# Optimization experiments

Hardware: AMD Instinct MI355X
Metric: run time of the kernel (lower is better)

The kernel has to match this reference:

```python
import jax, jax.numpy as jnp
import numpy as np
from jax import lax

EPS = 1e-5  # BatchNorm eps (inference mode: running_mean=m, running_var=v)
DN = ('NCDHW', 'OIDHW', 'NCDHW')


def _conv_bn_relu(x, W, b, g, bt, m, v, pad):
    y = lax.conv_general_dilated(x, W, window_strides=(1, 1, 1), padding=pad,
                                 dimension_numbers=DN)
    y = y + b[None, :, None, None, None]
    scale = g / jnp.sqrt(v + EPS)
    y = (y - m[None, :, None, None, None]) * scale[None, :, None, None, None] \
        + bt[None, :, None, None, None]
    return jax.nn.relu(y)


def _cal_patt(k, q, v):
    # spatial non-local attention over H*W, independently per (n, c, d)
    N, C, D, H, W = q.shape
    qf = q.reshape(N, C, D, H * W)
    kf = k.reshape(N, C, D, H * W)
    vf = v.reshape(N, C, D, H * W)
    # sigma[n,c,d,i,j] = q_i * k_j ; softmax over j ; out[j] = sum_i v_i * r_ij
    sigma = qf[..., :, None] * kf[..., None, :]          # [N,C,D,HW,HW]
    r = jax.nn.softmax(sigma, axis=-1)
    out = jnp.einsum('ncdi,ncdij->ncdj', vf, r)
    return out.reshape(N, C, D, H, W)


def _cal_datt(k, q, v):
    # temporal non-local attention over D, independently per (n, c, h, w)
    N, C, D, H, W = q.shape
    qf = jnp.transpose(q, (0, 1, 3, 4, 2))               # [N,C,H,W,D]
    kf = jnp.transpose(k, (0, 1, 3, 4, 2))
    vf = jnp.transpose(v, (0, 1, 3, 4, 2))
    sigma = qf[..., :, None] * kf[..., None, :]          # [N,C,H,W,D,D]
    r = jax.nn.softmax(sigma, axis=-1)
    out = jnp.einsum('nchwi,nchwij->nchwj', vf, r)
    return jnp.transpose(out, (0, 1, 4, 2, 3))           # back to [N,C,D,H,W]


def setup_inputs() -> dict:
    key = jax.random.key(0)
    ks = jax.random.split(key, 8)
    C, Cc = 512, 64  # features_, features_//compress
    N, D, H, W = 2, 8, 16, 16
    f32 = jnp.float32

    def bn(c):
        return (jnp.ones((c,), f32), jnp.zeros((c,), f32),
                jnp.zeros((c,), f32), jnp.ones((c,), f32))

    x = jax.random.normal(ks[0], (N, C, D, H, W), f32)
    Wq = jax.random.normal(ks[1], (Cc, C, 1, 1, 1), f32) * 0.04
    Wk = jax.random.normal(ks[2], (Cc, C, 1, 1, 1), f32) * 0.04
    Wv = jax.random.normal(ks[3], (Cc, C, 1, 1, 1), f32) * 0.04
    Ws = jax.random.normal(ks[4], (C, Cc, 3, 3, 3), f32) * 0.02
    Wd = jax.random.normal(ks[5], (C, Cc, 3, 3, 3), f32) * 0.02
    gq, btq, mq, vq = bn(Cc)
    gk, btk, mk, vk = bn(Cc)
    gv, btv, mv, vv = bn(Cc)
    gs, bts, ms, vs = bn(C)
    gd, btd, md, vd = bn(C)
    return dict(
        x=x, gama=jnp.float32(0.5),
        Wq=Wq, bq=jnp.zeros((Cc,), f32), gq=gq, btq=btq, mq=mq, vq=vq,
        Wk=Wk, bk=jnp.zeros((Cc,), f32), gk=gk, btk=btk, mk=mk, vk=vk,
        Wv=Wv, bv=jnp.zeros((Cc,), f32), gv=gv, btv=btv, mv=mv, vv=vv,
        Ws=Ws, bs=jnp.zeros((C,), f32), gs=gs, bts=bts, ms=ms, vs=vs,
        Wd=Wd, bd=jnp.zeros((C,), f32), gd=gd, btd=btd, md=md, vd=vd,
    )


def reference(x, gama,
              Wq, bq, gq, btq, mq, vq,
              Wk, bk, gk, btk, mk, vk,
              Wv, bv, gv, btv, mv, vv,
              Ws, bs, gs, bts, ms, vs,
              Wd, bd, gd, btd, md, vd):
    P0 = [(0, 0)] * 3
    P1 = [(1, 1)] * 3
    v_x = _conv_bn_relu(x, Wv, bv, gv, btv, mv, vv, P0)
    k_x = _conv_bn_relu(x, Wk, bk, gk, btk, mk, vk, P0)
    q_x = _conv_bn_relu(x, Wq, bq, gq, btq, mq, vq, P0)
    # name == 'st': both spatial and temporal attention branches
    Patt = _cal_patt(k_x, q_x, v_x)
    Patt_c = _conv_bn_relu(Patt, Ws, bs, gs, bts, ms, vs, P1)
    Datt = _cal_datt(k_x, q_x, v_x)
    Datt_c = _conv_bn_relu(Datt, Wd, bd, gd, btd, md, vd, P1)
    return gama * (Datt_c + Patt_c) + x
```

## Files before the change

### kernel.cpp

```cpp
#include <hip/hip_runtime.h>
#include <cmath>

#define EPSBN 1e-5f

namespace {
constexpr int C_IN = 512;
constexpr int CC   = 64;
constexpr int CD   = 8;
constexpr int HW   = 256;
constexpr int DHW  = CD * HW;
constexpr int QSZ  = 2 * CC * DHW;

constexpr int PG    = 18 * 18;
constexpr int GPLN  = PG * 8;
constexpr int PADSZ = 2 * 10 * 8 * GPLN;
constexpr int WTSZ  = 27 * 512 * 64;
constexpr int PSTR  = 1448;

typedef __attribute__((ext_vector_type(8))) short bf16x8;
typedef __attribute__((ext_vector_type(4))) float f32x4;
typedef __attribute__((ext_vector_type(16))) float f32x16;

typedef unsigned int u32_g __attribute__((address_space(1)));
typedef unsigned int u32_l __attribute__((address_space(3)));

__device__ inline unsigned short f2bf(float f) {
    unsigned u = __float_as_uint(f);
    return (unsigned short)((u + 0x7fffu + ((u >> 16) & 1u)) >> 16);
}
}

__global__ __launch_bounds__(256) void prep_kernel(
    const float* __restrict__ Ws, const float* __restrict__ Wd,
    const float* __restrict__ Wq, const float* __restrict__ Wk,
    const float* __restrict__ Wv,
    const float* __restrict__ bs, const float* __restrict__ gs,
    const float* __restrict__ bts, const float* __restrict__ ms,
    const float* __restrict__ vs,
    const float* __restrict__ bd, const float* __restrict__ gd,
    const float* __restrict__ btd, const float* __restrict__ md,
    const float* __restrict__ vd,
    uint4* __restrict__ pads, unsigned short* __restrict__ Wt,
    unsigned short* __restrict__ Wqkv, float2* __restrict__ BNc)
{
    int bid = blockIdx.x;
    int t = threadIdx.x;
    if (bid < 405) {
        pads[bid * 256 + t] = make_uint4(0, 0, 0, 0);
    } else if (bid < 1429) {
        int b2 = bid - 405;
        int b  = b2 >> 9;
        int co = b2 & 511;
        const float* W = b ? Wd : Ws;
        int cog = co >> 6, co_l = co & 63;
        unsigned short* o = Wt + (size_t)b * WTSZ;
        for (int k = t; k < 27 * 64; k += 256) {
            int tap = k >> 6, ci = k & 63;
            int kd = tap / 9, tapk = tap - kd * 9;
            int half = ci >> 5, cl = ci & 31;
            int cig = cl >> 4, ci16 = cl & 15;
            float w = W[((size_t)co * 64 + ci) * 27 + tap];
            int chunk = ((cog * 2 + half) * 3 + kd) * 2 + cig;
            o[(size_t)chunk * 9216 + tapk * 1024 + co_l * 16 + ci16] = f2bf(w);
        }
    } else if (bid < 1621) {
        int co = bid - 1429;
        const float* W = co < 64 ? Wq : co < 128 ? Wk : Wv;
        int c = co & 63;
        for (int ci = t; ci < 512; ci += 256)
            Wqkv[(size_t)co * 512 + ci] = f2bf(W[(size_t)c * 512 + ci]);
    } else {
        int gid = (bid - 1621) * 256 + t;
        if (gid < 1024) {
            int br = gid >> 9, co = gid & 511;
            float s, o;
            if (br == 0) {
                s = gs[co] * rsqrtf(vs[co] + EPSBN);
                o = (bs[co] - ms[co]) * s + bts[co];
            } else {
                s = gd[co] * rsqrtf(vd[co] + EPSBN);
                o = (bd[co] - md[co]) * s + btd[co];
            }
            BNc[gid] = make_float2(s, o);
        }
    }
}

__global__ __launch_bounds__(256) void qkv_gemm_kernel(
    const float* __restrict__ x, const unsigned short* __restrict__ Wqkv,
    const float* __restrict__ bq, const float* __restrict__ gq,
    const float* __restrict__ btq, const float* __restrict__ mq,
    const float* __restrict__ vq,
    const float* __restrict__ bk, const float* __restrict__ gk,
    const float* __restrict__ btk, const float* __restrict__ mk,
    const float* __restrict__ vk,
    const float* __restrict__ bv, const float* __restrict__ gv,
    const float* __restrict__ btv, const float* __restrict__ mv,
    const float* __restrict__ vv,
    float* __restrict__ outq, float* __restrict__ outk, float* __restrict__ outv)
{
    int bid = blockIdx.x;
    int n = bid >> 7, p0 = (bid & 127) * 16;

    __shared__ __align__(16) unsigned short xs[16 * 512];
    int t = threadIdx.x;

    const float* xb = x + ((size_t)n * C_IN) * DHW + p0;
#pragma unroll
    for (int pass = 0; pass < 8; ++pass) {
        int idx = pass * 256 + t;
        int ci = idx >> 2, pq = idx & 3;
        float4 v4 = *reinterpret_cast<const float4*>(xb + (size_t)ci * DHW + pq * 4);
        float arr[4] = {v4.x, v4.y, v4.z, v4.w};
#pragma unroll
        for (int u = 0; u < 4; ++u) {
            int pos = pq * 4 + u;
            int boff = pos * 1024 + ((ci * 2) ^ ((pos & 7) << 4));
            *reinterpret_cast<unsigned short*>(
                reinterpret_cast<char*>(xs) + boff) = f2bf(arr[u]);
        }
    }
    __syncthreads();

    int wid = t >> 6, lane = t & 63;
    int l15 = lane & 15, l4 = lane >> 4;
    int mh = wid * 3;
    int pos = l15;

    bf16x8 bfr[16];
    const char* xsb = reinterpret_cast<const char*>(xs) + pos * 1024;
    int swz = (pos & 7) << 4;
#pragma unroll
    for (int kk = 0; kk < 16; ++kk)
        bfr[kk] = *reinterpret_cast<const bf16x8*>(xsb + ((kk * 64 + l4 * 16) ^ swz));

    f32x4 acc[3];
#pragma unroll
    for (int i = 0; i < 3; ++i) acc[i] = (f32x4){0.f, 0.f, 0.f, 0.f};

#pragma unroll
    for (int i = 0; i < 3; ++i) {
        const unsigned short* wrow =
            Wqkv + ((size_t)(mh + i) * 16 + l15) * 512 + l4 * 8;
#pragma unroll
        for (int kk = 0; kk < 16; ++kk) {
            bf16x8 af = *reinterpret_cast<const bf16x8*>(wrow + kk * 32);
            acc[i] = __builtin_amdgcn_mfma_f32_16x16x32_bf16(af, bfr[kk], acc[i], 0, 0, 0);
        }
    }

#pragma unroll
    for (int i = 0; i < 3; ++i) {
        int mf = mh + i;
        int br = mf >> 2;
        const float* bb  = br == 0 ? bq  : br == 1 ? bk  : bv;
        const float* gg  = br == 0 ? gq  : br == 1 ? gk  : gv;
        const float* bt  = br == 0 ? btq : br == 1 ? btk : btv;
        const float* mm  = br == 0 ? mq  : br == 1 ? mk  : mv;
        const float* vvp = br == 0 ? vq  : br == 1 ? vk  : vv;
        float*       op  = br == 0 ? outq : br == 1 ? outk : outv;
        int cb = (mf & 3) * 16 + l4 * 4;
#pragma unroll
        for (int r = 0; r < 4; ++r) {
            int c = cb + r;
            float s = gg[c] * rsqrtf(vvp[c] + EPSBN);
            float val = (acc[i][r] + bb[c] - mm[c]) * s + bt[c];
            op[((size_t)(n * CC + c)) * DHW + p0 + pos] = fmaxf(val, 0.f);
        }
    }
}

__global__ __launch_bounds__(256) void att_kernel(
    const float* __restrict__ q, const float* __restrict__ k,
    const float* __restrict__ v,
    unsigned short* __restrict__ Pp, unsigned short* __restrict__ Dp)
{
    __shared__ float sk[256], sq[256], sw[256], red[4];
    int t = threadIdx.x;
    int bid = blockIdx.x;

    if (bid < 1024) {
        int n = bid >> 9, c = (bid >> 3) & 63, d = bid & 7;
        size_t base = (size_t)bid * HW;
        float kt = k[base + t];
        float qt = q[base + t];
        float vt = v[base + t];
        sk[t] = kt;
        sq[t] = qt;

        float m = kt;
#pragma unroll
        for (int off = 32; off >= 1; off >>= 1)
            m = fmaxf(m, __shfl_xor(m, off));
        if ((t & 63) == 0) red[t >> 6] = m;
        __syncthreads();
        float kmax = fmaxf(fmaxf(red[0], red[1]), fmaxf(red[2], red[3]));

        float qkm = qt * kmax;
        float d0 = 0.f, d1 = 0.f, d2 = 0.f, d3 = 0.f;
        for (int j = 0; j < 256; j += 4) {
            d0 += __expf(fmaf(qt, sk[j + 0], -qkm));
            d1 += __expf(fmaf(qt, sk[j + 1], -qkm));
            d2 += __expf(fmaf(qt, sk[j + 2], -qkm));
            d3 += __expf(fmaf(qt, sk[j + 3], -qkm));
        }
        float den = (d0 + d1) + (d2 + d3);
        sw[t] = vt / den;
        __syncthreads();

        float kjm = kt - kmax;
        float o0 = 0.f, o1 = 0.f, o2 = 0.f, o3 = 0.f;
        for (int i = 0; i < 256; i += 4) {
            o0 += sw[i + 0] * __expf(sq[i + 0] * kjm);
            o1 += sw[i + 1] * __expf(sq[i + 1] * kjm);
            o2 += sw[i + 2] * __expf(sq[i + 2] * kjm);
            o3 += sw[i + 3] * __expf(sq[i + 3] * kjm);
        }
        float o = (o0 + o1) + (o2 + o3);

        int h = t >> 4, w = t & 15;
        size_t dst = ((((size_t)(n * 10 + d + 1) * 8 + (c >> 3)) * PG)
                      + (h + 1) * 18 + (w + 1)) * 8 + (c & 7);
        Pp[dst] = f2bf(o);
    } else {
        int g = (bid - 1024) * 256 + t;
        int nc = g >> 8, hw = g & 255;
        int n = nc >> 6, c = nc & 63;
        size_t base = (size_t)nc * DHW + hw;

        float qv[8], kv[8], vv_[8];
#pragma unroll
        for (int d = 0; d < 8; ++d) {
            qv[d]  = q[base + d * HW];
            kv[d]  = k[base + d * HW];
            vv_[d] = v[base + d * HW];
        }
        float kmax = 0.f;
#pragma unroll
        for (int d = 0; d < 8; ++d) kmax = fmaxf(kmax, kv[d]);

        float wgt[8];
#pragma unroll
        for (int i = 0; i < 8; ++i) {
            float den = 0.f, qkm = qv[i] * kmax;
#pragma unroll
            for (int j = 0; j < 8; ++j)
                den += __expf(fmaf(qv[i], kv[j], -qkm));
            wgt[i] = vv_[i] / den;
        }
        int h = hw >> 4, w = hw & 15;
#pragma unroll
        for (int j = 0; j < 8; ++j) {
            float o = 0.f, kjm = kv[j] - kmax;
#pragma unroll
            for (int i = 0; i < 8; ++i)
                o += wgt[i] * __expf(qv[i] * kjm);
            size_t dst = ((((size_t)(n * 10 + j + 1) * 8 + (c >> 3)) * PG)
                          + (h + 1) * 18 + (w + 1)) * 8 + (c & 7);
            Dp[dst] = f2bf(o);
        }
    }
}

__global__ __launch_bounds__(256, 1) void conv_fused_kernel(
    const unsigned short* __restrict__ Pp, const unsigned short* __restrict__ Dp,
    const unsigned short* __restrict__ Wt,
    const float2* __restrict__ BNc,
    const float* __restrict__ x, const float* __restrict__ gama,
    float* __restrict__ out)
{
    int bid = blockIdx.x;
    int cog = bid & 7;
    int pgb = (bid >> 3) & 1;
    int sl  = bid >> 4;
    int n = sl >> 3, d = sl & 7;

    __shared__ __align__(16) unsigned short lds_in[2 * 12 * PSTR];
    __shared__ __align__(16) unsigned short lds_w[2 * 18432];

    int t = threadIdx.x;
    int wid = t >> 6, lane = t & 63;
    int ph = wid & 1, br = wid >> 1;
    int col  = lane & 31;
    int wcol = lane & 15;
    int hl   = (lane >> 4) & 1;
    int ks   = lane >> 5;

    f32x16 acc[2][2];
#pragma unroll
    for (int m = 0; m < 2; ++m)
#pragma unroll
        for (int p = 0; p < 2; ++p)
#pragma unroll
            for (int r = 0; r < 16; ++r)
                acc[m][p][r] = 0.f;

#define DMAW(c_) do {                                                         \
    const int ch_ = (((cog * 2 + ((c_) / 6)) * 3 + (((c_) % 6) >> 1)) * 2     \
                     + ((c_) & 1)) * 9216;                                    \
    _Pragma("unroll")                                                         \
    for (int j = 0; j < 9; ++j) {                                             \
        int base = j * 2048 + wid * 512;                                      \
        const unsigned short* s0 = (base < 9216)                              \
            ? (Wt + ch_ + base)                                               \
            : (Wt + WTSZ + ch_ + (base - 9216));                              \
        __builtin_amdgcn_global_load_lds(                                     \
            (const u32_g*)(s0 + lane * 8),                                    \
            (u32_l*)(lds_w + ((c_) & 1) * 18432 + base), 16, 0, 0);           \
    }                                                                         \
} while (0)

#define COMPUTE(c_) do {                                                      \
    const int kd_ = ((c_) % 6) >> 1, cig_ = (c_) & 1;                         \
    const unsigned short* wb_ = lds_w + ((c_) & 1) * 18432 + br * 9216;       \
    const unsigned short* bp_ = lds_in + br * (12 * PSTR)                     \
                                + (kd_ * 4 + cig_ * 2 + ks) * PSTR;           \
    _Pragma("unroll")                                                         \
    for (int tapk = 0; tapk < 9; ++tapk) {                                    \
        const int kh_ = tapk / 3, kw_ = tapk % 3;                             \
        bf16x8 a0 = *(const bf16x8*)(wb_ + tapk * 1024 + col * 16 + ks * 8);  \
        bf16x8 a1 = *(const bf16x8*)(wb_ + tapk * 1024 + 512 + col * 16       \
                                     + ks * 8);                               \
        bf16x8 b0 = *(const bf16x8*)(bp_ + ((ph * 4 + hl + kh_) * 18          \
                                     + wcol + kw_) * 8);                      \
        bf16x8 b1 = *(const bf16x8*)(bp_ + ((ph * 4 + 2 + hl + kh_) * 18      \
                                     + wcol + kw_) * 8);                      \
        acc[0][0] = __builtin_amdgcn_mfma_f32_32x32x16_bf16(a0, b0,           \
                        acc[0][0], 0, 0, 0);                                  \
        acc[0][1] = __builtin_amdgcn_mfma_f32_32x32x16_bf16(a0, b1,           \
                        acc[0][1], 0, 0, 0);                                  \
        acc[1][0] = __builtin_amdgcn_mfma_f32_32x32x16_bf16(a1, b0,           \
                        acc[1][0], 0, 0, 0);                                  \
        acc[1][1] = __builtin_amdgcn_mfma_f32_32x32x16_bf16(a1, b1,           \
                        acc[1][1], 0, 0, 0);                                  \
    }                                                                         \
} while (0)

#pragma unroll
    for (int i = 0; i < 17; ++i) {
        int idx = i * 256 + t;
        if (idx < 4320) {
            int b2 = idx >= 2160 ? 1 : 0;
            int sub = idx - b2 * 2160;
            int pl = sub / 180, rem = sub - pl * 180;
            const uint4* s = reinterpret_cast<const uint4*>(
                (b2 ? Dp : Pp)
                + (size_t)((n * 10 + d + (pl >> 2)) * 8 + (pl & 3)) * GPLN
                + pgb * 1152) + rem;
            reinterpret_cast<uint4*>(lds_in)[b2 * 2172 + pl * 181 + rem] = *s;
        }
    }
    DMAW(0);
    __syncthreads();

    uint4 streg[17];

#pragma unroll
    for (int c = 0; c < 12; ++c) {
        if (c < 11) DMAW(c + 1);
        if (c == 5) {
#pragma unroll
            for (int i = 0; i < 17; ++i) {
                int idx = i * 256 + t;
                if (idx < 4320) {
                    int b2 = idx >= 2160 ? 1 : 0;
                    int sub = idx - b2 * 2160;
                    int pl = sub / 180, rem = sub - pl * 180;
                    streg[i] = *(reinterpret_cast<const uint4*>(
                        (b2 ? Dp : Pp)
                        + (size_t)((n * 10 + d + (pl >> 2)) * 8 + 4
                                   + (pl & 3)) * GPLN + pgb * 1152) + rem);
                }
            }
        }
        COMPUTE(c);
        __syncthreads();
        if (c == 5) {
#pragma unroll
            for (int i = 0; i < 17; ++i) {
                int idx = i * 256 + t;
                if (idx < 4320) {
                    int b2 = idx >= 2160 ? 1 : 0;
                    int sub = idx - b2 * 2160;
                    int pl = sub / 180, rem = sub - pl * 180;
                    reinterpret_cast<uint4*>(lds_in)[b2 * 2172 + pl * 181 + rem]
                        = streg[i];
                }
            }
            __syncthreads();
        }
    }

#undef DMAW
#undef COMPUTE

    float gm = gama[0];
    float* ep = reinterpret_cast<float*>(lds_w);

    if (br == 0) {
#pragma unroll
        for (int m = 0; m < 2; ++m)
#pragma unroll
            for (int p = 0; p < 2; ++p)
#pragma unroll
                for (int r = 0; r < 16; ++r) {
                    int row = (r & 3) + 8 * (r >> 2) + 4 * ks;
                    float2 c2 = BNc[cog * 64 + m * 32 + row];
                    float v = fmaxf(acc[m][p][r] * c2.x + c2.y, 0.f);
                    ep[ph * 4096 + (m * 32 + row) * 64 + p * 32 + col] = v;
                }
    }
    __syncthreads();
    if (br == 1) {
#pragma unroll
        for (int m = 0; m < 2; ++m)
#pragma unroll
            for (int p = 0; p < 2; ++p)
#pragma unroll
                for (int r = 0; r < 16; ++r) {
                    int row = (r & 3) + 8 * (r >> 2) + 4 * ks;
                    int co = cog * 64 + m * 32 + row;
                    float2 c2 = BNc[512 + co];
                    float rd = fmaxf(acc[m][p][r] * c2.x + c2.y, 0.f);
                    float rp = ep[ph * 4096 + (m * 32 + row) * 64 + p * 32 + col];
                    int pos = pgb * 128 + ph * 64 + p * 32 + col;
                    size_t oi = ((size_t)(n * 512 + co)) * 2048 + d * 256 + pos;
                    out[oi] = gm * (rp + rd) + x[oi];
                }
    }
}

extern "C" void kernel_launch(void* const* d_in, const int* in_sizes, int n_in,
                              void* d_out, int out_size, void* d_ws, size_t ws_size,
                              hipStream_t stream)
{
    const float* x    = (const float*)d_in[0];
    const float* gama = (const float*)d_in[1];
    const float* Wq  = (const float*)d_in[2];
    const float* bq  = (const float*)d_in[3];
    const float* gq  = (const float*)d_in[4];
    const float* btq = (const float*)d_in[5];
    const float* mq  = (const float*)d_in[6];
    const float* vq  = (const float*)d_in[7];
    const float* Wk  = (const float*)d_in[8];
    const float* bk  = (const float*)d_in[9];
    const float* gk  = (const float*)d_in[10];
    const float* btk = (const float*)d_in[11];
    const float* mk  = (const float*)d_in[12];
    const float* vk  = (const float*)d_in[13];
    const float* Wv  = (const float*)d_in[14];
    const float* bv  = (const float*)d_in[15];
    const float* gv  = (const float*)d_in[16];
    const float* btv = (const float*)d_in[17];
    const float* mv  = (const float*)d_in[18];
    const float* vv  = (const float*)d_in[19];
    const float* Ws  = (const float*)d_in[20];
    const float* bs  = (const float*)d_in[21];
    const float* gs  = (const float*)d_in[22];
    const float* bts = (const float*)d_in[23];
    const float* ms  = (const float*)d_in[24];
    const float* vs  = (const float*)d_in[25];
    const float* Wd  = (const float*)d_in[26];
    const float* bd  = (const float*)d_in[27];
    const float* gd  = (const float*)d_in[28];
    const float* btd = (const float*)d_in[29];
    const float* md  = (const float*)d_in[30];
    const float* vd  = (const float*)d_in[31];

    char* ws = (char*)d_ws;
    unsigned short* Pp   = (unsigned short*)ws;
    unsigned short* Dp   = Pp + PADSZ;
    unsigned short* Wt   = Dp + PADSZ;
    unsigned short* Wqkv = Wt + 2 * WTSZ;
    float* q = (float*)(ws + 5394432);
    float* k = q + QSZ;
    float* v = k + QSZ;
    float2* BNc = (float2*)(ws + 5394432 + 3 * 1048576);

    prep_kernel<<<1625, 256, 0, stream>>>(
        Ws, Wd, Wq, Wk, Wv,
        bs, gs, bts, ms, vs,
        bd, gd, btd, md, vd,
        (uint4*)Pp, Wt, Wqkv, BNc);

    qkv_gemm_kernel<<<256, 256, 0, stream>>>(
        x, Wqkv,
        bq, gq, btq, mq, vq,
        bk, gk, btk, mk, vk,
        bv, gv, btv, mv, vv,
        q, k, v);

    att_kernel<<<1152, 256, 0, stream>>>(q, k, v, Pp, Dp);

    conv_fused_kernel<<<256, 256, 0, stream>>>(
        Pp, Dp, Wt, BNc,
        x, gama, (float*)d_out);
}
```

Measured before the change: 69.72 us.

## Stage conv inputs via direct global-to-LDS loads and XOR-swizzle weight layout

Result: faster. 65.02 us (-6.7%).

```diff
diff --git a/kernel.cpp b/kernel.cpp
--- a/kernel.cpp
+++ b/kernel.cpp
@@ -15,7 +15,6 @@
 constexpr int GPLN  = PG * 8;
 constexpr int PADSZ = 2 * 10 * 8 * GPLN;
 constexpr int WTSZ  = 27 * 512 * 64;
-constexpr int PSTR  = 1448;
 
 typedef __attribute__((ext_vector_type(8))) short bf16x8;
 typedef __attribute__((ext_vector_type(4))) float f32x4;
@@ -53,15 +52,19 @@
         int co = b2 & 511;
         const float* W = b ? Wd : Ws;
         int cog = co >> 6, co_l = co & 63;
+        int r  = co_l & 31, hi = co_l >> 5;
         unsigned short* o = Wt + (size_t)b * WTSZ;
         for (int k = t; k < 27 * 64; k += 256) {
             int tap = k >> 6, ci = k & 63;
             int kd = tap / 9, tapk = tap - kd * 9;
             int half = ci >> 5, cl = ci & 31;
             int cig = cl >> 4, ci16 = cl & 15;
+            int ks = ci16 >> 3;
             float w = W[((size_t)co * 64 + ci) * 27 + tap];
             int chunk = ((cog * 2 + half) * 3 + kd) * 2 + cig;
-            o[(size_t)chunk * 9216 + tapk * 1024 + co_l * 16 + ci16] = f2bf(w);
+            int pg = (r * 2 + ks) ^ (r & 7);
+            o[(size_t)chunk * 9216 + tapk * 1024 + hi * 512
+              + pg * 8 + (ci16 & 7)] = f2bf(w);
         }
     } else if (bid < 1621) {
         int co = bid - 1429;
@@ -275,7 +278,7 @@
     int sl  = bid >> 4;
     int n = sl >> 3, d = sl & 7;
 
-    __shared__ __align__(16) unsigned short lds_in[2 * 12 * PSTR];
+    __shared__ __align__(16) unsigned short lds_in[24 * 1536];
     __shared__ __align__(16) unsigned short lds_w[2 * 18432];
 
     int t = threadIdx.x;
@@ -285,6 +288,7 @@
     int wcol = lane & 15;
     int hl   = (lane >> 4) & 1;
     int ks   = lane >> 5;
+    int gA   = ((col * 2 + ks) ^ (col & 7)) * 8;
 
     f32x16 acc[2][2];
 #pragma unroll
@@ -294,6 +298,22 @@
 #pragma unroll
             for (int r = 0; r < 16; ++r)
                 acc[m][p][r] = 0.f;
+
+#define ISTAGE(hf_) do {                                                      \
+    _Pragma("unroll")                                                         \
+    for (int pc = 0; pc < 24; ++pc) {                                         \
+        const unsigned short* sb = ((pc >= 12) ? Dp : Pp)                     \
+            + ((size_t)((n * 10 + d + ((pc % 12) >> 2)) * 8 + (hf_) * 4       \
+                        + ((pc % 12) & 3))) * GPLN + pgb * 1152;              \
+        _Pragma("unroll")                                                     \
+        for (int j = 0; j < 3; ++j) {                                         \
+            if (((pc * 3 + j) & 3) == wid)                                    \
+                __builtin_amdgcn_global_load_lds(                             \
+                    (const u32_g*)(sb + j * 512 + lane * 8),                  \
+                    (u32_l*)(lds_in + pc * 1536 + j * 512), 16, 0, 0);        \
+        }                                                                     \
+    }                                                                         \
+} while (0)
 
 #define DMAW(c_) do {                                                         \
     const int ch_ = (((cog * 2 + ((c_) / 6)) * 3 + (((c_) % 6) >> 1)) * 2     \
@@ -313,14 +333,13 @@
 #define COMPUTE(c_) do {                                                      \
     const int kd_ = ((c_) % 6) >> 1, cig_ = (c_) & 1;                         \
     const unsigned short* wb_ = lds_w + ((c_) & 1) * 18432 + br * 9216;       \
-    const unsigned short* bp_ = lds_in + br * (12 * PSTR)                     \
-                                + (kd_ * 4 + cig_ * 2 + ks) * PSTR;           \
+    const unsigned short* bp_ = lds_in + br * (12 * 1536)                     \
+                                + (kd_ * 4 + cig_ * 2 + ks) * 1536;           \
     _Pragma("unroll")                                                         \
     for (int tapk = 0; tapk < 9; ++tapk) {                                    \
         const int kh_ = tapk / 3, kw_ = tapk % 3;                             \
-        bf16x8 a0 = *(const bf16x8*)(wb_ + tapk * 1024 + col * 16 + ks * 8);  \
-        bf16x8 a1 = *(const bf16x8*)(wb_ + tapk * 1024 + 512 + col * 16       \
-                                     + ks * 8);                               \
+        bf16x8 a0 = *(const bf16x8*)(wb_ + tapk * 1024 + gA);                 \
+        bf16x8 a1 = *(const bf16x8*)(wb_ + tapk * 1024 + 512 + gA);           \
         bf16x8 b0 = *(const bf16x8*)(bp_ + ((ph * 4 + hl + kh_) * 18          \
                                      + wcol + kw_) * 8);                      \
         bf16x8 b1 = *(const bf16x8*)(bp_ + ((ph * 4 + 2 + hl + kh_) * 18      \
@@ -336,61 +355,22 @@
     }                                                                         \
 } while (0)
 
-#pragma unroll
-    for (int i = 0; i < 17; ++i) {
-        int idx = i * 256 + t;
-        if (idx < 4320) {
-            int b2 = idx >= 2160 ? 1 : 0;
-            int sub = idx - b2 * 2160;
-            int pl = sub / 180, rem = sub - pl * 180;
-            const uint4* s = reinterpret_cast<const uint4*>(
-                (b2 ? Dp : Pp)
-                + (size_t)((n * 10 + d + (pl >> 2)) * 8 + (pl & 3)) * GPLN
-                + pgb * 1152) + rem;
-            reinterpret_cast<uint4*>(lds_in)[b2 * 2172 + pl * 181 + rem] = *s;
-        }
-    }
+    ISTAGE(0);
     DMAW(0);
     __syncthreads();
 
-    uint4 streg[17];
-
 #pragma unroll
     for (int c = 0; c < 12; ++c) {
         if (c < 11) DMAW(c + 1);
-        if (c == 5) {
-#pragma unroll
-            for (int i = 0; i < 17; ++i) {
-                int idx = i * 256 + t;
-                if (idx < 4320) {
-                    int b2 = idx >= 2160 ? 1 : 0;
-                    int sub = idx - b2 * 2160;
-                    int pl = sub / 180, rem = sub - pl * 180;
-                    streg[i] = *(reinterpret_cast<const uint4*>(
-                        (b2 ? Dp : Pp)
-                        + (size_t)((n * 10 + d + (pl >> 2)) * 8 + 4
-                                   + (pl & 3)) * GPLN + pgb * 1152) + rem);
-                }
-            }
-        }
         COMPUTE(c);
         __syncthreads();
         if (c == 5) {
-#pragma unroll
-            for (int i = 0; i < 17; ++i) {
-                int idx = i * 256 + t;
-                if (idx < 4320) {
-                    int b2 = idx >= 2160 ? 1 : 0;
-                    int sub = idx - b2 * 2160;
-                    int pl = sub / 180, rem = sub - pl * 180;
-                    reinterpret_cast<uint4*>(lds_in)[b2 * 2172 + pl * 181 + rem]
-                        = streg[i];
-                }
-            }
+            ISTAGE(1);
             __syncthreads();
         }
     }
 
+#undef ISTAGE
 #undef DMAW
 #undef COMPUTE
 
```
